# Performance work log

Measured on AMD Instinct MI355X. Metric: run time of the kernel, lower is better.

## Reference

```python
import jax, jax.numpy as jnp
import numpy as np

B, T, C, H = 4, 2048, 1024, 16
D = C // H  # head dim = 64


def setup_inputs() -> dict:
    key = jax.random.key(0)
    k_x, k_wa, k_ba, k_wp, k_bp = jax.random.split(key, 5)
    s = 1.0 / np.sqrt(C)
    return {
        "x": jax.random.normal(k_x, (B, T, C), dtype=jnp.float32),
        "w_attn": jax.random.uniform(k_wa, (C, 3 * C), minval=-s, maxval=s, dtype=jnp.float32),
        "b_attn": jax.random.uniform(k_ba, (3 * C,), minval=-s, maxval=s, dtype=jnp.float32),
        "w_proj": jax.random.uniform(k_wp, (C, C), minval=-s, maxval=s, dtype=jnp.float32),
        "b_proj": jax.random.uniform(k_bp, (C,), minval=-s, maxval=s, dtype=jnp.float32),
    }


def reference(x, w_attn, b_attn, w_proj, b_proj):
    b, t, c = x.shape
    qkv = x @ w_attn + b_attn  # [b, t, 3c]
    q, k, v = jnp.split(qkv, 3, axis=-1)
    # [b, h, t, d]
    q = q.reshape(b, t, H, D).transpose(0, 2, 1, 3)
    k = k.reshape(b, t, H, D).transpose(0, 2, 1, 3)
    v = v.reshape(b, t, H, D).transpose(0, 2, 1, 3)
    scale = 1.0 / np.sqrt(D)
    logits = jnp.einsum("bhqd,bhkd->bhqk", q, k) * scale
    causal = jnp.tril(jnp.ones((t, t), dtype=bool))
    logits = jnp.where(causal, logits, jnp.finfo(logits.dtype).min)
    attn = jax.nn.softmax(logits, axis=-1)
    y = jnp.einsum("bhqk,bhkd->bhqd", attn, v)
    y = y.transpose(0, 2, 1, 3).reshape(b, t, c)
    return y @ w_proj + b_proj
```

## Files before the change

kernel.cpp:

```cpp
#include <hip/hip_runtime.h>


using u16 = unsigned short;
using u32 = unsigned int;
using bf16x8 = __attribute__((ext_vector_type(8))) __bf16;
using f32x4  = __attribute__((ext_vector_type(4))) float;
using u16x8  = __attribute__((ext_vector_type(8))) u16;
using u16x4  = __attribute__((ext_vector_type(4))) u16;
using u32x2  = __attribute__((ext_vector_type(2))) u32;
using fvec4  = __attribute__((ext_vector_type(4))) float;

__device__ __forceinline__ u16 f2bf(float f) {
  u32 u = __builtin_bit_cast(u32, f);
  u32 r = (u + 0x7FFFu + ((u >> 16) & 1u)) >> 16;
  return (u16)r;
}

__device__ __forceinline__ u32 cvtpk(float lo, float hi) {
  u32 r;
  asm("v_cvt_pk_bf16_f32 %0, %1, %2" : "=v"(r) : "v"(lo), "v"(hi));
  return r;
}

__device__ __forceinline__ f32x4 mfma16(bf16x8 a, bf16x8 b, f32x4 c) {
  return __builtin_amdgcn_mfma_f32_16x16x32_bf16(a, b, c, 0, 0, 0);
}

__device__ __forceinline__ void gld16(const u16* g, u16* l) {
  __builtin_amdgcn_global_load_lds(
      (const __attribute__((address_space(1))) void*)g,
      (__attribute__((address_space(3))) void*)l, 16, 0, 0);
}

__device__ __forceinline__ void lgkm_barrier() {
  asm volatile("s_waitcnt lgkmcnt(0)" ::: "memory");
  __builtin_amdgcn_s_barrier();
  __builtin_amdgcn_sched_barrier(0);
}

__global__ __launch_bounds__(256) void conv_kernel(
    const float* __restrict__ in, u16* __restrict__ out) {
  const size_t i = ((size_t)blockIdx.x * 256 + threadIdx.x) * 8;
  fvec4 a = *(const fvec4*)(in + i);
  fvec4 b = *(const fvec4*)(in + i + 4);
  u16x8 h;
#pragma unroll
  for (int j = 0; j < 4; ++j) { h[j] = f2bf(a[j]); h[4 + j] = f2bf(b[j]); }
  *(u16x8*)(out + i) = h;
}

__global__ __launch_bounds__(256) void transpose_conv_kernel(
    const float* __restrict__ W, u16* __restrict__ Wt, int K, int N) {
  __shared__ float tile[32][33];
  const int n0 = blockIdx.x * 32, k0 = blockIdx.y * 32;
  const int tx = threadIdx.x, ty = threadIdx.y;
#pragma unroll
  for (int j = 0; j < 4; ++j)
    tile[ty + j * 8][tx] = W[(size_t)(k0 + ty + j * 8) * N + n0 + tx];
  __syncthreads();
#pragma unroll
  for (int j = 0; j < 4; ++j)
    Wt[(size_t)(n0 + ty + j * 8) * K + k0 + tx] = f2bf(tile[tx][ty + j * 8]);
}

template <bool QKV>
__global__ __launch_bounds__(256) void gemm_kernel(
    const u16* __restrict__ A, const u16* __restrict__ Bt,
    const float* __restrict__ bias, void* __restrict__ Cp,
    u16* __restrict__ vt, int M, int N, int K) {
  constexpr float SC = 0.18033688011112042f;
  __shared__ u16 As[128 * 32];
  __shared__ u16 Bs[128 * 32];
  const int tid = threadIdx.x;
  const int lane = tid & 63;
  const int w = tid >> 6;
  const int wm = (w >> 1) * 64, wn = (w & 1) * 64;
  const int l15 = lane & 15, l16 = lane >> 4;

  const u32 nwg = gridDim.x * gridDim.y;
  u32 f = blockIdx.y * gridDim.x + blockIdx.x;
  f = (f & 7) * (nwg >> 3) + (f >> 3);
  const long mbase = (long)(f / gridDim.x) * 128;
  const long nbase = (long)(f % gridDim.x) * 128;

  const int srow = tid >> 2, scol = (tid & 3) * 8;
  const u16* ga = A + (mbase + srow) * (long)K + scol;
  const u16* gb = Bt + (nbase + srow) * (long)K + scol;
  u16* lA0 = &As[tid * 8];
  u16* lA1 = &As[2048 + tid * 8];
  u16* lB0 = &Bs[tid * 8];
  u16* lB1 = &Bs[2048 + tid * 8];

  f32x4 acc[4][4] = {};

  for (int kb = 0; kb < K; kb += 32) {
    __syncthreads();
    gld16(ga + kb, lA0);
    gld16(ga + 64 * (long)K + kb, lA1);
    gld16(gb + kb, lB0);
    gld16(gb + 64 * (long)K + kb, lB1);
    __syncthreads();

    bf16x8 af[4], bfr[4];
#pragma unroll
    for (int i = 0; i < 4; ++i) af[i] = *(const bf16x8*)(&As[(wm + i * 16 + l15) * 32 + l16 * 8]);
#pragma unroll
    for (int j = 0; j < 4; ++j) bfr[j] = *(const bf16x8*)(&Bs[(wn + j * 16 + l15) * 32 + l16 * 8]);
#pragma unroll
    for (int i = 0; i < 4; ++i)
#pragma unroll
      for (int j = 0; j < 4; ++j)
        acc[i][j] = mfma16(af[i], bfr[j], acc[i][j]);
  }

  if constexpr (QKV) {
    const bool isv = (nbase >= 2048);
#pragma unroll
    for (int i = 0; i < 4; ++i) {
#pragma unroll
      for (int j = 0; j < 4; ++j) {
        const long m0 = mbase + wm + i * 16 + l16 * 4;
        const int n = (int)nbase + wn + j * 16 + l15;
        const float bv = bias[n];
        if (!isv) {
          u16* qkp = (u16*)Cp;
          const float sc = (n < 1024) ? SC : 1.0f;
#pragma unroll
          for (int r = 0; r < 4; ++r)
            qkp[(m0 + r) * 2048 + n] = f2bf((acc[i][j][r] + bv) * sc);
        } else {
          const int vc = n - 2048, hh = vc >> 6, dd = vc & 63;
          const int bb = (int)(m0 >> 11), t0 = (int)(m0 & 2047);
          u16x4 pk;
#pragma unroll
          for (int r = 0; r < 4; ++r) pk[r] = f2bf(acc[i][j][r] + bv);
          *(u16x4*)(vt + ((size_t)(bb * 16 + hh) * 64 + dd) * 2048 + t0) = pk;
        }
      }
    }
  } else {
#pragma unroll
    for (int i = 0; i < 4; ++i) {
#pragma unroll
      for (int j = 0; j < 4; ++j) {
        const long row0 = mbase + wm + i * 16 + l16 * 4;
        const long col = nbase + wn + j * 16 + l15;
        const float bv = bias[col];
#pragma unroll
        for (int r = 0; r < 4; ++r)
          ((float*)Cp)[(row0 + r) * (long)N + col] = acc[i][j][r] + bv;
      }
    }
  }
}

__global__ __launch_bounds__(256) void flash_kernel(
    const u16* __restrict__ qk, const u16* __restrict__ vt, u16* __restrict__ attn_out) {
  constexpr float MFIX = 4.0f;
  __shared__ u16 Ks[64][72];
  __shared__ u16 Vs[64][72];
  __shared__ u16 Ps[4][16][72];
  __shared__ float InvL[4][16];
  const int tid = threadIdx.x;
  const int lane = tid & 63, w = tid >> 6;
  const int l15 = lane & 15, l16 = lane >> 4;
  const u32 f = blockIdx.y * 16 + blockIdx.x;
  const int pair = (f >> 3) & 15;
  const int bh = (f & 7) + ((f >> 7) << 3);
  const int b = bh >> 4, h = bh & 15;
  const u16* qbase = qk + (size_t)b * 2048 * 2048 + h * 64;
  const u16* kbase = qbase + 1024;
  const u16* vbase = vt + (size_t)bh * 64 * 2048;
  u16* obase = attn_out + (size_t)b * 2048 * 1024 + h * 64;

  const int r0 = tid >> 3, c0 = (tid & 7) * 8;

  for (int half = 0; half < 2; ++half) {
    const int qt = half ? (31 - pair) : pair;
    const int nt = qt + 1;
    const int qr0 = qt * 64 + w * 16;
    const int qrow = qr0 + l15;

    const bf16x8 qf0 = *(const bf16x8*)(qbase + (size_t)qrow * 2048 + l16 * 8);
    const bf16x8 qf1 = *(const bf16x8*)(qbase + (size_t)qrow * 2048 + 32 + l16 * 8);

    f32x4 o[4] = {};
    float lsum = 0.f;

    u16x8 kreg[2], vreg[2];
    kreg[0] = *(const u16x8*)(kbase + (size_t)r0 * 2048 + c0);
    kreg[1] = *(const u16x8*)(kbase + (size_t)(r0 + 32) * 2048 + c0);
    vreg[0] = *(const u16x8*)(vbase + (size_t)r0 * 2048 + c0);
    vreg[1] = *(const u16x8*)(vbase + (size_t)(r0 + 32) * 2048 + c0);

    for (int kt = 0; kt < nt; ++kt) {
      const int kb = kt * 64;
      lgkm_barrier();
      *(u16x8*)(&Ks[r0][c0]) = kreg[0];
      *(u16x8*)(&Ks[r0 + 32][c0]) = kreg[1];
      *(u16x8*)(&Vs[r0][c0]) = vreg[0];
      *(u16x8*)(&Vs[r0 + 32][c0]) = vreg[1];
      lgkm_barrier();
      if (kt + 1 < nt) {
        const int nb = kb + 64;
        kreg[0] = *(const u16x8*)(kbase + (size_t)(nb + r0) * 2048 + c0);
        kreg[1] = *(const u16x8*)(kbase + (size_t)(nb + r0 + 32) * 2048 + c0);
        vreg[0] = *(const u16x8*)(vbase + (size_t)r0 * 2048 + nb + c0);
        vreg[1] = *(const u16x8*)(vbase + (size_t)(r0 + 32) * 2048 + nb + c0);
      }

      f32x4 s[4];
      __builtin_amdgcn_s_setprio(1);
#pragma unroll
      for (int ni = 0; ni < 4; ++ni) {
        bf16x8 k0 = *(const bf16x8*)(&Ks[ni * 16 + l15][l16 * 8]);
        bf16x8 k1 = *(const bf16x8*)(&Ks[ni * 16 + l15][32 + l16 * 8]);
        f32x4 t = {};
        t = mfma16(k0, qf0, t);
        t = mfma16(k1, qf1, t);
        s[ni] = t;
      }
      __builtin_amdgcn_s_setprio(0);

      if (kt == nt - 1) {
#pragma unroll
        for (int ni = 0; ni < 4; ++ni)
#pragma unroll
          for (int r = 0; r < 4; ++r)
            if (kb + ni * 16 + l16 * 4 + r > qrow) s[ni][r] = -1e30f;
      }

      float p[4][4];
      float ps = 0.f;
#pragma unroll
      for (int ni = 0; ni < 4; ++ni)
#pragma unroll
        for (int r = 0; r < 4; ++r) {
          p[ni][r] = exp2f(s[ni][r] - MFIX);
          ps += p[ni][r];
        }
      lsum += ps;

#pragma unroll
      for (int ni = 0; ni < 4; ++ni) {
        u32x2 pk;
        pk[0] = cvtpk(p[ni][0], p[ni][1]);
        pk[1] = cvtpk(p[ni][2], p[ni][3]);
        *(u32x2*)(&Ps[w][l15][ni * 16 + l16 * 4]) = pk;
      }

      __builtin_amdgcn_s_setprio(1);
#pragma unroll
      for (int ki = 0; ki < 2; ++ki) {
        bf16x8 pa = *(const bf16x8*)(&Ps[w][l15][ki * 32 + l16 * 8]);
#pragma unroll
        for (int ni = 0; ni < 4; ++ni) {
          bf16x8 vb = *(const bf16x8*)(&Vs[ni * 16 + l15][ki * 32 + l16 * 8]);
          o[ni] = mfma16(pa, vb, o[ni]);
        }
      }
      __builtin_amdgcn_s_setprio(0);
    }

    lsum += __shfl_xor(lsum, 16);
    lsum += __shfl_xor(lsum, 32);
    const float inv = 1.0f / lsum;
    if (l16 == 0) InvL[w][l15] = inv;
    float ir[4];
#pragma unroll
    for (int r = 0; r < 4; ++r) ir[r] = InvL[w][l16 * 4 + r];
#pragma unroll
    for (int r = 0; r < 4; ++r) {
      const int t = qr0 + l16 * 4 + r;
#pragma unroll
      for (int ni = 0; ni < 4; ++ni)
        obase[(size_t)t * 1024 + ni * 16 + l15] = f2bf(o[ni][r] * ir[r]);
    }
  }
}

extern "C" void kernel_launch(void* const* d_in, const int* in_sizes, int n_in,
                              void* d_out, int out_size, void* d_ws, size_t ws_size,
                              hipStream_t stream) {
  (void)in_sizes; (void)n_in; (void)out_size; (void)ws_size;
  const float* x      = (const float*)d_in[0];
  const float* w_attn = (const float*)d_in[1];
  const float* b_attn = (const float*)d_in[2];
  const float* w_proj = (const float*)d_in[3];
  const float* b_proj = (const float*)d_in[4];
  float* out = (float*)d_out;

  char* ws = (char*)d_ws;
  u16* qkbuf = (u16*)(ws);
  u16* vtbuf = (u16*)(ws + 33554432);
  u16* xbf   = (u16*)(ws + 50331648);
  u16* attnb = (u16*)(ws + 50331648);
  u16* wtA   = (u16*)(ws + 67108864);
  u16* wtP   = (u16*)(ws + 73400320);

  conv_kernel<<<4096, 256, 0, stream>>>(x, xbf);
  transpose_conv_kernel<<<dim3(3072 / 32, 1024 / 32), dim3(32, 8), 0, stream>>>(w_attn, wtA, 1024, 3072);
  transpose_conv_kernel<<<dim3(1024 / 32, 1024 / 32), dim3(32, 8), 0, stream>>>(w_proj, wtP, 1024, 1024);

  gemm_kernel<true><<<dim3(3072 / 128, 8192 / 128), 256, 0, stream>>>(
      xbf, wtA, b_attn, qkbuf, vtbuf, 8192, 3072, 1024);

  flash_kernel<<<dim3(16, 64), 256, 0, stream>>>(qkbuf, vtbuf, attnb);

  gemm_kernel<false><<<dim3(1024 / 128, 8192 / 128), 256, 0, stream>>>(
      attnb, wtP, b_proj, out, nullptr, 8192, 1024, 1024);
}
```

Before: 199.4 us.

## Double flash query tile to 128 rows per block and swizzle LDS tiles

Each wave of the flash kernel now handles 32 query rows instead of 16, so every K/V tile loaded into LDS is reused across twice as many MFMAs and the grid shrinks to 512 blocks with causal pairing over 16 query tiles. The padded LDS arrays are replaced by XOR-swizzled 128-byte rows to avoid bank conflicts without padding. Launch bounds request two blocks per CU. The larger tiles raise register use and halve block count, which may reduce occupancy and load balance.

```diff
diff --git a/kernel.cpp b/kernel.cpp
--- a/kernel.cpp
+++ b/kernel.cpp
@@ -36,6 +36,13 @@
   asm volatile("s_waitcnt lgkmcnt(0)" ::: "memory");
   __builtin_amdgcn_s_barrier();
   __builtin_amdgcn_sched_barrier(0);
+}
+
+__device__ __forceinline__ u16* swz(u16* base, int row, int colByte) {
+  return (u16*)((char*)base + row * 128 + (colByte ^ ((row & 7) << 4)));
+}
+__device__ __forceinline__ const u16* swzc(const u16* base, int row, int colByte) {
+  return (const u16*)((const char*)base + row * 128 + (colByte ^ ((row & 7) << 4)));
 }
 
 __global__ __launch_bounds__(256) void conv_kernel(
@@ -154,38 +161,45 @@
   }
 }
 
-__global__ __launch_bounds__(256) void flash_kernel(
+__global__ __launch_bounds__(256, 2) void flash_kernel(
     const u16* __restrict__ qk, const u16* __restrict__ vt, u16* __restrict__ attn_out) {
   constexpr float MFIX = 4.0f;
-  __shared__ u16 Ks[64][72];
-  __shared__ u16 Vs[64][72];
-  __shared__ u16 Ps[4][16][72];
-  __shared__ float InvL[4][16];
+  __shared__ u16 Ks[64 * 64];
+  __shared__ u16 Vs[64 * 64];
+  __shared__ u16 Ps[4 * 32 * 64];
+  __shared__ float InvL[4][32];
   const int tid = threadIdx.x;
   const int lane = tid & 63, w = tid >> 6;
   const int l15 = lane & 15, l16 = lane >> 4;
-  const u32 f = blockIdx.y * 16 + blockIdx.x;
-  const int pair = (f >> 3) & 15;
-  const int bh = (f & 7) + ((f >> 7) << 3);
+
+  const u32 i = blockIdx.y * 8 + blockIdx.x;
+  const int j = i >> 3;
+  const int bh = (i & 7) | ((j & 7) << 3);
+  const int pair = (int)(i >> 6);
   const int b = bh >> 4, h = bh & 15;
   const u16* qbase = qk + (size_t)b * 2048 * 2048 + h * 64;
   const u16* kbase = qbase + 1024;
   const u16* vbase = vt + (size_t)bh * 64 * 2048;
   u16* obase = attn_out + (size_t)b * 2048 * 1024 + h * 64;
+  u16* PsW = Ps + w * 32 * 64;
 
   const int r0 = tid >> 3, c0 = (tid & 7) * 8;
+  const int sco = ((c0 * 2) ^ ((r0 & 7) << 4)) >> 1;
 
   for (int half = 0; half < 2; ++half) {
-    const int qt = half ? (31 - pair) : pair;
-    const int nt = qt + 1;
-    const int qr0 = qt * 64 + w * 16;
-    const int qrow = qr0 + l15;
-
-    const bf16x8 qf0 = *(const bf16x8*)(qbase + (size_t)qrow * 2048 + l16 * 8);
-    const bf16x8 qf1 = *(const bf16x8*)(qbase + (size_t)qrow * 2048 + 32 + l16 * 8);
-
-    f32x4 o[4] = {};
-    float lsum = 0.f;
+    const int qt = half ? (15 - pair) : pair;
+    const int nt = 2 * qt + 2;
+    const int qr0 = qt * 128 + w * 32;
+
+    bf16x8 qa[2][2];
+#pragma unroll
+    for (int fq = 0; fq < 2; ++fq)
+#pragma unroll
+      for (int ks = 0; ks < 2; ++ks)
+        qa[fq][ks] = *(const bf16x8*)(qbase + (size_t)(qr0 + fq * 16 + l15) * 2048 + ks * 32 + l16 * 8);
+
+    f32x4 o[2][4] = {};
+    float lsum[2] = {0.f, 0.f};
 
     u16x8 kreg[2], vreg[2];
     kreg[0] = *(const u16x8*)(kbase + (size_t)r0 * 2048 + c0);
@@ -196,10 +210,10 @@
     for (int kt = 0; kt < nt; ++kt) {
       const int kb = kt * 64;
       lgkm_barrier();
-      *(u16x8*)(&Ks[r0][c0]) = kreg[0];
-      *(u16x8*)(&Ks[r0 + 32][c0]) = kreg[1];
-      *(u16x8*)(&Vs[r0][c0]) = vreg[0];
-      *(u16x8*)(&Vs[r0 + 32][c0]) = vreg[1];
+      *(u16x8*)(&Ks[r0 * 64 + sco]) = kreg[0];
+      *(u16x8*)(&Ks[(r0 + 32) * 64 + sco]) = kreg[1];
+      *(u16x8*)(&Vs[r0 * 64 + sco]) = vreg[0];
+      *(u16x8*)(&Vs[(r0 + 32) * 64 + sco]) = vreg[1];
       lgkm_barrier();
       if (kt + 1 < nt) {
         const int nb = kb + 64;
@@ -209,72 +223,91 @@
         vreg[1] = *(const u16x8*)(vbase + (size_t)(r0 + 32) * 2048 + nb + c0);
       }
 
-      f32x4 s[4];
+      f32x4 s[2][4];
       __builtin_amdgcn_s_setprio(1);
 #pragma unroll
       for (int ni = 0; ni < 4; ++ni) {
-        bf16x8 k0 = *(const bf16x8*)(&Ks[ni * 16 + l15][l16 * 8]);
-        bf16x8 k1 = *(const bf16x8*)(&Ks[ni * 16 + l15][32 + l16 * 8]);
-        f32x4 t = {};
-        t = mfma16(k0, qf0, t);
-        t = mfma16(k1, qf1, t);
-        s[ni] = t;
+        bf16x8 k0 = *(const bf16x8*)swzc(Ks, ni * 16 + l15, l16 * 16);
+        bf16x8 k1 = *(const bf16x8*)swzc(Ks, ni * 16 + l15, 64 + l16 * 16);
+        f32x4 t0 = {}, t1 = {};
+        t0 = mfma16(k0, qa[0][0], t0);
+        t0 = mfma16(k1, qa[0][1], t0);
+        t1 = mfma16(k0, qa[1][0], t1);
+        t1 = mfma16(k1, qa[1][1], t1);
+        s[0][ni] = t0;
+        s[1][ni] = t1;
       }
       __builtin_amdgcn_s_setprio(0);
 
-      if (kt == nt - 1) {
+      if (kb + 63 > qr0) {
+#pragma unroll
+        for (int fq = 0; fq < 2; ++fq) {
+          const int qrow = qr0 + fq * 16 + l15;
+#pragma unroll
+          for (int ni = 0; ni < 4; ++ni)
+#pragma unroll
+            for (int r = 0; r < 4; ++r)
+              if (kb + ni * 16 + l16 * 4 + r > qrow) s[fq][ni][r] = -1e30f;
+        }
+      }
+
+#pragma unroll
+      for (int fq = 0; fq < 2; ++fq) {
+        float ps = 0.f;
+        float p[4][4];
 #pragma unroll
         for (int ni = 0; ni < 4; ++ni)
 #pragma unroll
-          for (int r = 0; r < 4; ++r)
-            if (kb + ni * 16 + l16 * 4 + r > qrow) s[ni][r] = -1e30f;
-      }
-
-      float p[4][4];
-      float ps = 0.f;
-#pragma unroll
-      for (int ni = 0; ni < 4; ++ni)
-#pragma unroll
-        for (int r = 0; r < 4; ++r) {
-          p[ni][r] = exp2f(s[ni][r] - MFIX);
-          ps += p[ni][r];
+          for (int r = 0; r < 4; ++r) {
+            p[ni][r] = exp2f(s[fq][ni][r] - MFIX);
+            ps += p[ni][r];
+          }
+        lsum[fq] += ps;
+#pragma unroll
+        for (int ni = 0; ni < 4; ++ni) {
+          u32x2 pk;
+          pk[0] = cvtpk(p[ni][0], p[ni][1]);
+          pk[1] = cvtpk(p[ni][2], p[ni][3]);
+          *(u32x2*)swz(PsW, fq * 16 + l15, ni * 32 + l16 * 8) = pk;
         }
-      lsum += ps;
-
-#pragma unroll
-      for (int ni = 0; ni < 4; ++ni) {
-        u32x2 pk;
-        pk[0] = cvtpk(p[ni][0], p[ni][1]);
-        pk[1] = cvtpk(p[ni][2], p[ni][3]);
-        *(u32x2*)(&Ps[w][l15][ni * 16 + l16 * 4]) = pk;
       }
 
       __builtin_amdgcn_s_setprio(1);
 #pragma unroll
       for (int ki = 0; ki < 2; ++ki) {
-        bf16x8 pa = *(const bf16x8*)(&Ps[w][l15][ki * 32 + l16 * 8]);
-#pragma unroll
-        for (int ni = 0; ni < 4; ++ni) {
-          bf16x8 vb = *(const bf16x8*)(&Vs[ni * 16 + l15][ki * 32 + l16 * 8]);
-          o[ni] = mfma16(pa, vb, o[ni]);
+        bf16x8 vb[4];
+#pragma unroll
+        for (int ni = 0; ni < 4; ++ni)
+          vb[ni] = *(const bf16x8*)swzc(Vs, ni * 16 + l15, ki * 64 + l16 * 16);
+#pragma unroll
+        for (int fq = 0; fq < 2; ++fq) {
+          bf16x8 pa = *(const bf16x8*)swzc(PsW, fq * 16 + l15, ki * 64 + l16 * 16);
+#pragma unroll
+          for (int ni = 0; ni < 4; ++ni)
+            o[fq][ni] = mfma16(pa, vb[ni], o[fq][ni]);
         }
       }
       __builtin_amdgcn_s_setprio(0);
     }
 
-    lsum += __shfl_xor(lsum, 16);
-    lsum += __shfl_xor(lsum, 32);
-    const float inv = 1.0f / lsum;
-    if (l16 == 0) InvL[w][l15] = inv;
-    float ir[4];
-#pragma unroll
-    for (int r = 0; r < 4; ++r) ir[r] = InvL[w][l16 * 4 + r];
-#pragma unroll
-    for (int r = 0; r < 4; ++r) {
-      const int t = qr0 + l16 * 4 + r;
-#pragma unroll
-      for (int ni = 0; ni < 4; ++ni)
-        obase[(size_t)t * 1024 + ni * 16 + l15] = f2bf(o[ni][r] * ir[r]);
+#pragma unroll
+    for (int fq = 0; fq < 2; ++fq) {
+      float ls = lsum[fq];
+      ls += __shfl_xor(ls, 16);
+      ls += __shfl_xor(ls, 32);
+      if (l16 == 0) InvL[w][fq * 16 + l15] = 1.0f / ls;
+    }
+    __builtin_amdgcn_wave_barrier();
+#pragma unroll
+    for (int fq = 0; fq < 2; ++fq) {
+#pragma unroll
+      for (int r = 0; r < 4; ++r) {
+        const float ir = InvL[w][fq * 16 + l16 * 4 + r];
+        const int t = qr0 + fq * 16 + l16 * 4 + r;
+#pragma unroll
+        for (int ni = 0; ni < 4; ++ni)
+          obase[(size_t)t * 1024 + ni * 16 + l15] = f2bf(o[fq][ni][r] * ir);
+      }
     }
   }
 }
@@ -305,7 +338,7 @@
   gemm_kernel<true><<<dim3(3072 / 128, 8192 / 128), 256, 0, stream>>>(
       xbf, wtA, b_attn, qkbuf, vtbuf, 8192, 3072, 1024);
 
-  flash_kernel<<<dim3(16, 64), 256, 0, stream>>>(qkbuf, vtbuf, attnb);
+  flash_kernel<<<dim3(8, 64), 256, 0, stream>>>(qkbuf, vtbuf, attnb);
 
   gemm_kernel<false><<<dim3(1024 / 128, 8192 / 128), 256, 0, stream>>>(
       attnb, wtP, b_proj, out, nullptr, 8192, 1024, 1024);
```

After: 188.8 us. 5.3% less time.
